# Optimization experiments

Hardware: AMD Instinct MI355X
Metric: run time of the kernel (lower is better)

Reference implementation:

```python
import jax, jax.numpy as jnp
import numpy as np

B, D_IN, T = 8, 1024, 2048
CODEBOOK_SIZE, CODEBOOK_DIM = 8192, 8
EPS = 1e-12  # F.normalize default eps


def _l2_normalize(x, axis=-1):
    # matches torch F.normalize: x / max(||x||_2, eps)
    n = jnp.sqrt(jnp.sum(x * x, axis=axis, keepdims=True))
    return x / jnp.maximum(n, EPS)


def setup_inputs() -> dict:
    key = jax.random.key(0)
    k_z, k_wi, k_bi, k_wo, k_bo, k_cb = jax.random.split(key, 6)
    z = jax.random.normal(k_z, (B, D_IN, T), dtype=jnp.float32)
    # weight_norm(Conv1d) is a reparameterization; the effective weight is a
    # plain [out, in] matrix for a kernel_size=1 conv.
    w_in = jax.random.normal(k_wi, (CODEBOOK_DIM, D_IN), dtype=jnp.float32) * (1.0 / np.sqrt(D_IN))
    b_in = jax.random.normal(k_bi, (CODEBOOK_DIM,), dtype=jnp.float32) * 0.01
    w_out = jax.random.normal(k_wo, (D_IN, CODEBOOK_DIM), dtype=jnp.float32) * (1.0 / np.sqrt(CODEBOOK_DIM))
    b_out = jax.random.normal(k_bo, (D_IN,), dtype=jnp.float32) * 0.01
    codebook = jax.random.normal(k_cb, (CODEBOOK_SIZE, CODEBOOK_DIM), dtype=jnp.float32)
    return {"z": z, "w_in": w_in, "b_in": b_in, "w_out": w_out, "b_out": b_out, "codebook": codebook}


def reference(z, w_in, b_in, w_out, b_out, codebook):
    b, _, t = z.shape
    # in_project: 1x1 conv == matmul over channel dim
    z_e = jnp.einsum('od,bdt->bot', w_in, z) + b_in[None, :, None]  # [B, cd, T]

    # decode_latents
    enc = z_e.transpose(0, 2, 1).reshape(b * t, CODEBOOK_DIM)  # (b t) d
    enc_n = _l2_normalize(enc, axis=1)
    cb_n = _l2_normalize(codebook, axis=1)
    # dist = ||e||^2 - 2 e @ c^T + ||c||^2  (materializes [B*T, K] as original)
    dist = (jnp.sum(enc_n * enc_n, axis=1, keepdims=True)
            - 2.0 * (enc_n @ cb_n.T)
            + jnp.sum(cb_n * cb_n, axis=1)[None, :])
    indices = jnp.argmax(-dist, axis=1).reshape(b, t)  # [B, T] int
    # decode_code uses the UNnormalized codebook
    z_q = codebook[indices].transpose(0, 2, 1)  # [B, cd, T]

    # straight-through estimator
    z_q_st = z_e + jax.lax.stop_gradient(z_q - z_e)
    out = jnp.einsum('od,bdt->bot', w_out, z_q_st) + b_out[None, :, None]  # [B, D, T]

    commit_loss = jnp.zeros((b,), dtype=z.dtype)
    codebook_loss = jnp.zeros((b,), dtype=z.dtype)
    return (out, commit_loss, codebook_loss, indices, z_e)
```

## Files before the change

kernel.cpp:

```cpp
#include <hip/hip_runtime.h>
#include <math.h>

static constexpr int Bq  = 8;
static constexpr int DIN = 1024;
static constexpr int TTT = 2048;
static constexpr int KCB = 8192;

static constexpr int NCH = 64;
static constexpr int CPC = 128;

static constexpr size_t OUT_OFS  = 0;
static constexpr size_t LOSS_OFS = (size_t)Bq * DIN * TTT;
static constexpr size_t IDX_OFS  = LOSS_OFS + 16;
static constexpr size_t ZE_OFS   = IDX_OFS + (size_t)Bq * TTT;

static constexpr size_t WS_CBN  = 0;
static constexpr size_t WS_C2   = 65536;
static constexpr size_t WS_WT   = 73728;
static constexpr size_t WS_ENC  = 81920;
static constexpr size_t WS_PART = 212992;
static constexpr size_t WS_IDXI = WS_PART + (size_t)2 * NCH * 16384;

__global__ __launch_bounds__(256) void k0_prep(
    const float* __restrict__ w_in, const float* __restrict__ codebook,
    float* __restrict__ ws, float* __restrict__ out)
{
  int tid = blockIdx.x * 256 + threadIdx.x;
  if (tid < KCB) {
    const float4* cp = (const float4*)(codebook + (size_t)tid * 8);
    float4 a = cp[0], b = cp[1];
    float v[8] = {a.x, a.y, a.z, a.w, b.x, b.y, b.z, b.w};
    float n2 = 0.f;
#pragma unroll
    for (int o = 0; o < 8; o++) n2 = fmaf(v[o], v[o], n2);
    float dn = fmaxf(sqrtf(n2), 1e-12f);
    float u[8];
    float s2 = 0.f;
#pragma unroll
    for (int o = 0; o < 8; o++) { u[o] = v[o] / dn; s2 = fmaf(u[o], u[o], s2); }
    float4* wp = (float4*)(ws + WS_CBN + (size_t)tid * 8);
    wp[0] = make_float4(u[0], u[1], u[2], u[3]);
    wp[1] = make_float4(u[4], u[5], u[6], u[7]);
    ws[WS_C2 + tid] = 0.5f * s2;
  } else if (tid < KCB + DIN) {
    int d = tid - KCB;
#pragma unroll
    for (int o = 0; o < 8; o++) ws[WS_WT + (size_t)d * 8 + o] = w_in[(size_t)o * DIN + d];
  } else if (tid < KCB + DIN + 16) {
    out[LOSS_OFS + (tid - KCB - DIN)] = 0.f;
  }
}

__global__ __launch_bounds__(512) void k1_proj_in(
    const float* __restrict__ z, const float* __restrict__ b_in,
    float* __restrict__ ws, float* __restrict__ out)
{
  __shared__ __align__(16) float lds[16384];
  int tid = threadIdx.x;
  int bx = blockIdx.x;
  int b = bx >> 5;
  int t0 = (bx & 31) << 6;
  {
    const float4* src = (const float4*)(ws + WS_WT);
    float4* dst = (float4*)lds;
#pragma unroll
    for (int i = 0; i < 4; i++) dst[tid + 512 * i] = src[tid + 512 * i];
  }
  __syncthreads();
  int tt = tid & 15;
  int dg = tid >> 4;
  const float* zb = z + (size_t)b * DIN * TTT + t0 + (tt << 2);
  float4 acc[8];
#pragma unroll
  for (int o = 0; o < 8; o++) acc[o] = make_float4(0.f, 0.f, 0.f, 0.f);
  int dbase = dg << 5;
  const float4* wl = (const float4*)lds;
#pragma unroll 8
  for (int i = 0; i < 32; i++) {
    int d = dbase + i;
    float4 zv = *(const float4*)(zb + (size_t)d * TTT);
    float4 w0 = wl[d * 2 + 0];
    float4 w1 = wl[d * 2 + 1];
#define ACC1(o, wsc)                                    \
    acc[o].x = fmaf(wsc, zv.x, acc[o].x);               \
    acc[o].y = fmaf(wsc, zv.y, acc[o].y);               \
    acc[o].z = fmaf(wsc, zv.z, acc[o].z);               \
    acc[o].w = fmaf(wsc, zv.w, acc[o].w);
    ACC1(0, w0.x) ACC1(1, w0.y) ACC1(2, w0.z) ACC1(3, w0.w)
    ACC1(4, w1.x) ACC1(5, w1.y) ACC1(6, w1.z) ACC1(7, w1.w)
#undef ACC1
  }
  __syncthreads();
  {
    float4* pl = (float4*)lds;
#pragma unroll
    for (int o = 0; o < 8; o++) pl[dg * 128 + o * 16 + tt] = acc[o];
  }
  __syncthreads();
  int o = tid >> 6;
  int t = tid & 63;
  float s = 0.f;
#pragma unroll
  for (int g = 0; g < 32; g++) s += lds[g * 512 + o * 64 + t];
  s += b_in[o];
  out[ZE_OFS + ((size_t)b * 8 + o) * TTT + t0 + t] = s;
  ws[WS_ENC + ((size_t)(b * TTT + t0 + t)) * 8 + o] = s;
}

__global__ __launch_bounds__(256) void k2_scan(float* __restrict__ ws)
{
  __shared__ __align__(16) float4 scb[CPC * 2];
  __shared__ float sch[CPC];
  int tid = threadIdx.x;
  int rb = blockIdx.x >> 6;
  int ch = blockIdx.x & 63;
  int k0 = ch << 7;
  if (tid < CPC) {
    const float4* src = (const float4*)(ws + WS_CBN + (size_t)(k0 + tid) * 8);
    scb[tid * 2]     = src[0];
    scb[tid * 2 + 1] = src[1];
    sch[tid] = ws[WS_C2 + k0 + tid];
  }
  int rbase = (rb << 11) + tid;

#define DECL_ROW(j) float4 m##j##a, m##j##b; float b##j = 3.4e38f; int i##j = 0;
  DECL_ROW(0) DECL_ROW(1) DECL_ROW(2) DECL_ROW(3)
  DECL_ROW(4) DECL_ROW(5) DECL_ROW(6) DECL_ROW(7)
#undef DECL_ROW

#define LOAD_ROW(j) {                                                         \
    int r = rbase + (j << 8);                                                 \
    const float4* ep = (const float4*)(ws + WS_ENC + (size_t)r * 8);          \
    float4 a = ep[0], c = ep[1];                                              \
    float n2 = 0.f;                                                           \
    n2 = fmaf(a.x, a.x, n2); n2 = fmaf(a.y, a.y, n2);                         \
    n2 = fmaf(a.z, a.z, n2); n2 = fmaf(a.w, a.w, n2);                         \
    n2 = fmaf(c.x, c.x, n2); n2 = fmaf(c.y, c.y, n2);                         \
    n2 = fmaf(c.z, c.z, n2); n2 = fmaf(c.w, c.w, n2);                         \
    float dn = fmaxf(sqrtf(n2), 1e-12f);                                      \
    m##j##a.x = -(a.x / dn); m##j##a.y = -(a.y / dn);                         \
    m##j##a.z = -(a.z / dn); m##j##a.w = -(a.w / dn);                         \
    m##j##b.x = -(c.x / dn); m##j##b.y = -(c.y / dn);                         \
    m##j##b.z = -(c.z / dn); m##j##b.w = -(c.w / dn); }
  LOAD_ROW(0) LOAD_ROW(1) LOAD_ROW(2) LOAD_ROW(3)
  LOAD_ROW(4) LOAD_ROW(5) LOAD_ROW(6) LOAD_ROW(7)
#undef LOAD_ROW

  __syncthreads();
#pragma unroll 4
  for (int k = 0; k < CPC; k++) {
    float4 c0 = scb[2 * k];
    float4 c1 = scb[2 * k + 1];
    float cc = sch[k];
    int kk = k0 + k;
#define STEP(j) {                                                             \
    float s = cc;                                                             \
    s = fmaf(m##j##a.x, c0.x, s); s = fmaf(m##j##a.y, c0.y, s);               \
    s = fmaf(m##j##a.z, c0.z, s); s = fmaf(m##j##a.w, c0.w, s);               \
    s = fmaf(m##j##b.x, c1.x, s); s = fmaf(m##j##b.y, c1.y, s);               \
    s = fmaf(m##j##b.z, c1.z, s); s = fmaf(m##j##b.w, c1.w, s);               \
    if (s < b##j) { b##j = s; i##j = kk; } }
    STEP(0) STEP(1) STEP(2) STEP(3) STEP(4) STEP(5) STEP(6) STEP(7)
#undef STEP
  }
  float2* part = (float2*)(ws + WS_PART);
#define STORE_ROW(j) \
  part[(size_t)ch * 16384 + rbase + (j << 8)] = make_float2(b##j, __int_as_float(i##j));
  STORE_ROW(0) STORE_ROW(1) STORE_ROW(2) STORE_ROW(3)
  STORE_ROW(4) STORE_ROW(5) STORE_ROW(6) STORE_ROW(7)
#undef STORE_ROW
}

__global__ __launch_bounds__(256) void k2b_reduce(float* __restrict__ ws, float* __restrict__ out)
{
  int r = blockIdx.x * 256 + threadIdx.x;
  const float2* part = (const float2*)(ws + WS_PART);
  float best = 3.4e38f;
  int bi = 0;
#pragma unroll 8
  for (int ch = 0; ch < NCH; ch++) {
    float2 p = part[(size_t)ch * 16384 + r];
    if (p.x < best) { best = p.x; bi = __float_as_int(p.y); }
  }
  out[IDX_OFS + r] = (float)bi;
  ((int*)(ws + WS_IDXI))[r] = bi;
}

__global__ __launch_bounds__(256) void k3_proj_out(
    const float* __restrict__ codebook, const float* __restrict__ w_out,
    const float* __restrict__ b_out, const float* __restrict__ ws,
    float* __restrict__ out)
{
  int bx = blockIdx.x;
  int b = bx >> 7;
  int th = (bx >> 6) & 1;
  int dt = bx & 63;
  int tid = threadIdx.x;
  int t = (th << 10) + (tid << 2);
  const int* idxp = (const int*)(ws + WS_IDXI);
  int4 id = *(const int4*)(idxp + b * TTT + t);
  const float4* cbp = (const float4*)codebook;
  float4 c00 = cbp[(size_t)id.x * 2], c01 = cbp[(size_t)id.x * 2 + 1];
  float4 c10 = cbp[(size_t)id.y * 2], c11 = cbp[(size_t)id.y * 2 + 1];
  float4 c20 = cbp[(size_t)id.z * 2], c21 = cbp[(size_t)id.z * 2 + 1];
  float4 c30 = cbp[(size_t)id.w * 2], c31 = cbp[(size_t)id.w * 2 + 1];
  int d0 = dt << 4;
#pragma unroll 4
  for (int dd = 0; dd < 16; dd++) {
    int d = d0 + dd;
    const float* wr = w_out + (size_t)d * 8;
    float w0 = wr[0], w1 = wr[1], w2 = wr[2], w3 = wr[3];
    float w4 = wr[4], w5 = wr[5], w6 = wr[6], w7 = wr[7];
    float bb = b_out[d];
#define DOT8(lo, hi)                                                          \
    fmaf(w7, hi.w, fmaf(w6, hi.z, fmaf(w5, hi.y, fmaf(w4, hi.x,              \
    fmaf(w3, lo.w, fmaf(w2, lo.z, fmaf(w1, lo.y, fmaf(w0, lo.x, bb))))))))
    float4 r;
    r.x = DOT8(c00, c01);
    r.y = DOT8(c10, c11);
    r.z = DOT8(c20, c21);
    r.w = DOT8(c30, c31);
#undef DOT8
    *(float4*)(out + OUT_OFS + ((size_t)b * DIN + d) * TTT + t) = r;
  }
}

extern "C" void kernel_launch(void* const* d_in, const int* in_sizes, int n_in,
                              void* d_out, int out_size, void* d_ws, size_t ws_size,
                              hipStream_t stream) {
  const float* z        = (const float*)d_in[0];
  const float* w_in     = (const float*)d_in[1];
  const float* b_in     = (const float*)d_in[2];
  const float* w_out    = (const float*)d_in[3];
  const float* b_out    = (const float*)d_in[4];
  const float* codebook = (const float*)d_in[5];
  float* out = (float*)d_out;
  float* ws  = (float*)d_ws;

  k0_prep<<<dim3(37), dim3(256), 0, stream>>>(w_in, codebook, ws, out);
  k1_proj_in<<<dim3(256), dim3(512), 0, stream>>>(z, b_in, ws, out);
  k2_scan<<<dim3(512), dim3(256), 0, stream>>>(ws);
  k2b_reduce<<<dim3(64), dim3(256), 0, stream>>>(ws, out);
  k3_proj_out<<<dim3(1024), dim3(256), 0, stream>>>(codebook, w_out, b_out, ws, out);
}
```

Measured before the change: 196.1 us.

## Retile projection and scan kernels, hoist normalization, pre-gather codebook rows

The input projection now runs 1024 blocks of 256 threads over 16-timestep tiles. It reads transposed weights straight from global memory instead of staging them in LDS. Encoder-row normalization moves into a separate small kernel, so the scan kernel only loads pre-normalized rows. The scan handles 4 rows per thread over twice as many blocks to raise occupancy. The reduce kernel gathers the selected codebook rows into a contiguous buffer, so the output projection reads them coalesced rather than via indices. This adds an extra launch and extra workspace traffic in exchange for more parallelism in the earlier stages.

New measurement: 206.8 us. 5.5% more time.

```diff
diff --git a/kernel.cpp b/kernel.cpp
--- a/kernel.cpp
+++ b/kernel.cpp
@@ -18,7 +18,8 @@
 static constexpr size_t WS_C2   = 65536;
 static constexpr size_t WS_WT   = 73728;
 static constexpr size_t WS_ENC  = 81920;
-static constexpr size_t WS_PART = 212992;
+static constexpr size_t WS_Q    = 212992;
+static constexpr size_t WS_PART = 344064;
 static constexpr size_t WS_IDXI = WS_PART + (size_t)2 * NCH * 16384;
 
 __global__ __launch_bounds__(256) void k0_prep(
@@ -51,36 +52,28 @@
   }
 }
 
-__global__ __launch_bounds__(512) void k1_proj_in(
+__global__ __launch_bounds__(256, 4) void k1_proj_in(
     const float* __restrict__ z, const float* __restrict__ b_in,
     float* __restrict__ ws, float* __restrict__ out)
 {
-  __shared__ __align__(16) float lds[16384];
+  __shared__ __align__(16) float lds[64 * 136];
   int tid = threadIdx.x;
   int bx = blockIdx.x;
-  int b = bx >> 5;
-  int t0 = (bx & 31) << 6;
-  {
-    const float4* src = (const float4*)(ws + WS_WT);
-    float4* dst = (float4*)lds;
-#pragma unroll
-    for (int i = 0; i < 4; i++) dst[tid + 512 * i] = src[tid + 512 * i];
-  }
-  __syncthreads();
-  int tt = tid & 15;
-  int dg = tid >> 4;
+  int b = bx >> 7;
+  int t0 = (bx & 127) << 4;
+  int dg = tid >> 2;
+  int tt = tid & 3;
   const float* zb = z + (size_t)b * DIN * TTT + t0 + (tt << 2);
+  const float4* wt = (const float4*)(ws + WS_WT);
   float4 acc[8];
 #pragma unroll
   for (int o = 0; o < 8; o++) acc[o] = make_float4(0.f, 0.f, 0.f, 0.f);
-  int dbase = dg << 5;
-  const float4* wl = (const float4*)lds;
-#pragma unroll 8
-  for (int i = 0; i < 32; i++) {
-    int d = dbase + i;
+#pragma unroll 4
+  for (int i = 0; i < 16; i++) {
+    int d = dg + (i << 6);
     float4 zv = *(const float4*)(zb + (size_t)d * TTT);
-    float4 w0 = wl[d * 2 + 0];
-    float4 w1 = wl[d * 2 + 1];
+    float4 w0 = wt[d * 2 + 0];
+    float4 w1 = wt[d * 2 + 1];
 #define ACC1(o, wsc)                                    \
     acc[o].x = fmaf(wsc, zv.x, acc[o].x);               \
     acc[o].y = fmaf(wsc, zv.y, acc[o].y);               \
@@ -90,24 +83,41 @@
     ACC1(4, w1.x) ACC1(5, w1.y) ACC1(6, w1.z) ACC1(7, w1.w)
 #undef ACC1
   }
+  {
+    float* pl = lds + dg * 136 + (tt << 2);
+#pragma unroll
+    for (int o = 0; o < 8; o++) *(float4*)(pl + o * 16) = acc[o];
+  }
   __syncthreads();
-  {
-    float4* pl = (float4*)lds;
-#pragma unroll
-    for (int o = 0; o < 8; o++) pl[dg * 128 + o * 16 + tt] = acc[o];
-  }
-  __syncthreads();
-  int o = tid >> 6;
-  int t = tid & 63;
-  float s = 0.f;
-#pragma unroll
-  for (int g = 0; g < 32; g++) s += lds[g * 512 + o * 64 + t];
-  s += b_in[o];
-  out[ZE_OFS + ((size_t)b * 8 + o) * TTT + t0 + t] = s;
-  ws[WS_ENC + ((size_t)(b * TTT + t0 + t)) * 8 + o] = s;
-}
-
-__global__ __launch_bounds__(256) void k2_scan(float* __restrict__ ws)
+  if (tid < 128) {
+    int o = tid >> 4;
+    int t = tid & 15;
+    float s = 0.f;
+#pragma unroll
+    for (int g = 0; g < 64; g++) s += lds[g * 136 + (o << 4) + t];
+    s += b_in[o];
+    out[ZE_OFS + ((size_t)b * 8 + o) * TTT + t0 + t] = s;
+    ws[WS_ENC + ((size_t)b * TTT + t0 + t) * 8 + o] = s;
+  }
+}
+
+__global__ __launch_bounds__(256) void k1b_norm(float* __restrict__ ws)
+{
+  int r = blockIdx.x * 256 + threadIdx.x;
+  float4* ep = (float4*)(ws + WS_ENC + (size_t)r * 8);
+  float4 a = ep[0], c = ep[1];
+  float n2 = 0.f;
+  n2 = fmaf(a.x, a.x, n2); n2 = fmaf(a.y, a.y, n2);
+  n2 = fmaf(a.z, a.z, n2); n2 = fmaf(a.w, a.w, n2);
+  n2 = fmaf(c.x, c.x, n2); n2 = fmaf(c.y, c.y, n2);
+  n2 = fmaf(c.z, c.z, n2); n2 = fmaf(c.w, c.w, n2);
+  float dn = fmaxf(sqrtf(n2), 1e-12f);
+  a.x = -(a.x / dn); a.y = -(a.y / dn); a.z = -(a.z / dn); a.w = -(a.w / dn);
+  c.x = -(c.x / dn); c.y = -(c.y / dn); c.z = -(c.z / dn); c.w = -(c.w / dn);
+  ep[0] = a; ep[1] = c;
+}
+
+__global__ __launch_bounds__(256, 4) void k2_scan(float* __restrict__ ws)
 {
   __shared__ __align__(16) float4 scb[CPC * 2];
   __shared__ float sch[CPC];
@@ -121,29 +131,15 @@
     scb[tid * 2 + 1] = src[1];
     sch[tid] = ws[WS_C2 + k0 + tid];
   }
-  int rbase = (rb << 11) + tid;
+  int rbase = (rb << 10) + tid;
 
 #define DECL_ROW(j) float4 m##j##a, m##j##b; float b##j = 3.4e38f; int i##j = 0;
   DECL_ROW(0) DECL_ROW(1) DECL_ROW(2) DECL_ROW(3)
-  DECL_ROW(4) DECL_ROW(5) DECL_ROW(6) DECL_ROW(7)
 #undef DECL_ROW
-
 #define LOAD_ROW(j) {                                                         \
-    int r = rbase + (j << 8);                                                 \
-    const float4* ep = (const float4*)(ws + WS_ENC + (size_t)r * 8);          \
-    float4 a = ep[0], c = ep[1];                                              \
-    float n2 = 0.f;                                                           \
-    n2 = fmaf(a.x, a.x, n2); n2 = fmaf(a.y, a.y, n2);                         \
-    n2 = fmaf(a.z, a.z, n2); n2 = fmaf(a.w, a.w, n2);                         \
-    n2 = fmaf(c.x, c.x, n2); n2 = fmaf(c.y, c.y, n2);                         \
-    n2 = fmaf(c.z, c.z, n2); n2 = fmaf(c.w, c.w, n2);                         \
-    float dn = fmaxf(sqrtf(n2), 1e-12f);                                      \
-    m##j##a.x = -(a.x / dn); m##j##a.y = -(a.y / dn);                         \
-    m##j##a.z = -(a.z / dn); m##j##a.w = -(a.w / dn);                         \
-    m##j##b.x = -(c.x / dn); m##j##b.y = -(c.y / dn);                         \
-    m##j##b.z = -(c.z / dn); m##j##b.w = -(c.w / dn); }
+    const float4* ep = (const float4*)(ws + WS_ENC + (size_t)(rbase + (j << 8)) * 8); \
+    m##j##a = ep[0]; m##j##b = ep[1]; }
   LOAD_ROW(0) LOAD_ROW(1) LOAD_ROW(2) LOAD_ROW(3)
-  LOAD_ROW(4) LOAD_ROW(5) LOAD_ROW(6) LOAD_ROW(7)
 #undef LOAD_ROW
 
   __syncthreads();
@@ -160,18 +156,18 @@
     s = fmaf(m##j##b.x, c1.x, s); s = fmaf(m##j##b.y, c1.y, s);               \
     s = fmaf(m##j##b.z, c1.z, s); s = fmaf(m##j##b.w, c1.w, s);               \
     if (s < b##j) { b##j = s; i##j = kk; } }
-    STEP(0) STEP(1) STEP(2) STEP(3) STEP(4) STEP(5) STEP(6) STEP(7)
+    STEP(0) STEP(1) STEP(2) STEP(3)
 #undef STEP
   }
   float2* part = (float2*)(ws + WS_PART);
 #define STORE_ROW(j) \
   part[(size_t)ch * 16384 + rbase + (j << 8)] = make_float2(b##j, __int_as_float(i##j));
   STORE_ROW(0) STORE_ROW(1) STORE_ROW(2) STORE_ROW(3)
-  STORE_ROW(4) STORE_ROW(5) STORE_ROW(6) STORE_ROW(7)
 #undef STORE_ROW
 }
 
-__global__ __launch_bounds__(256) void k2b_reduce(float* __restrict__ ws, float* __restrict__ out)
+__global__ __launch_bounds__(256) void k2b_reduce(
+    const float* __restrict__ codebook, float* __restrict__ ws, float* __restrict__ out)
 {
   int r = blockIdx.x * 256 + threadIdx.x;
   const float2* part = (const float2*)(ws + WS_PART);
@@ -184,12 +180,15 @@
   }
   out[IDX_OFS + r] = (float)bi;
   ((int*)(ws + WS_IDXI))[r] = bi;
+  const float4* cb = (const float4*)codebook;
+  float4* q = (float4*)(ws + WS_Q + (size_t)r * 8);
+  q[0] = cb[(size_t)bi * 2];
+  q[1] = cb[(size_t)bi * 2 + 1];
 }
 
 __global__ __launch_bounds__(256) void k3_proj_out(
-    const float* __restrict__ codebook, const float* __restrict__ w_out,
-    const float* __restrict__ b_out, const float* __restrict__ ws,
-    float* __restrict__ out)
+    const float* __restrict__ w_out, const float* __restrict__ b_out,
+    const float* __restrict__ ws, float* __restrict__ out)
 {
   int bx = blockIdx.x;
   int b = bx >> 7;
@@ -197,13 +196,11 @@
   int dt = bx & 63;
   int tid = threadIdx.x;
   int t = (th << 10) + (tid << 2);
-  const int* idxp = (const int*)(ws + WS_IDXI);
-  int4 id = *(const int4*)(idxp + b * TTT + t);
-  const float4* cbp = (const float4*)codebook;
-  float4 c00 = cbp[(size_t)id.x * 2], c01 = cbp[(size_t)id.x * 2 + 1];
-  float4 c10 = cbp[(size_t)id.y * 2], c11 = cbp[(size_t)id.y * 2 + 1];
-  float4 c20 = cbp[(size_t)id.z * 2], c21 = cbp[(size_t)id.z * 2 + 1];
-  float4 c30 = cbp[(size_t)id.w * 2], c31 = cbp[(size_t)id.w * 2 + 1];
+  const float4* qp = (const float4*)(ws + WS_Q + ((size_t)b * TTT + t) * 8);
+  float4 c00 = qp[0], c01 = qp[1];
+  float4 c10 = qp[2], c11 = qp[3];
+  float4 c20 = qp[4], c21 = qp[5];
+  float4 c30 = qp[6], c31 = qp[7];
   int d0 = dt << 4;
 #pragma unroll 4
   for (int dd = 0; dd < 16; dd++) {
@@ -238,8 +235,9 @@
   float* ws  = (float*)d_ws;
 
   k0_prep<<<dim3(37), dim3(256), 0, stream>>>(w_in, codebook, ws, out);
-  k1_proj_in<<<dim3(256), dim3(512), 0, stream>>>(z, b_in, ws, out);
-  k2_scan<<<dim3(512), dim3(256), 0, stream>>>(ws);
-  k2b_reduce<<<dim3(64), dim3(256), 0, stream>>>(ws, out);
-  k3_proj_out<<<dim3(1024), dim3(256), 0, stream>>>(codebook, w_out, b_out, ws, out);
-}
+  k1_proj_in<<<dim3(1024), dim3(256), 0, stream>>>(z, b_in, ws, out);
+  k1b_norm<<<dim3(64), dim3(256), 0, stream>>>(ws);
+  k2_scan<<<dim3(1024), dim3(256), 0, stream>>>(ws);
+  k2b_reduce<<<dim3(64), dim3(256), 0, stream>>>(codebook, ws, out);
+  k3_proj_out<<<dim3(1024), dim3(256), 0, stream>>>(w_out, b_out, ws, out);
+}
```
